# Kernel optimization log

Measured on AMD Instinct MI355X. Metric: run time of the kernel, lower is better.

## Reference

```python
import jax, jax.numpy as jnp
import numpy as np
from jax import lax

D_MODEL = 512
N_HEADS = 8
D_HEAD = D_MODEL // N_HEADS
MAX_LANDMARKS = 100


def setup_inputs() -> dict:
    key = jax.random.key(0)
    ks = jax.random.split(key, 12)
    B, L, D = 16, 8192, D_MODEL
    s = 1.0 / np.sqrt(D)
    return {
        "mamba_output": jax.random.normal(ks[0], (B, L, D), jnp.float32),
        "hawkes_skip": jax.random.normal(ks[1], (B, L, D), jnp.float32),
        "hawkes_weights": jax.random.uniform(ks[2], (B, L), jnp.float32),
        "Wq": jax.random.uniform(ks[3], (D, D), jnp.float32, -s, s),
        "bq": jax.random.uniform(ks[4], (D,), jnp.float32, -s, s),
        "Wk": jax.random.uniform(ks[5], (D, D), jnp.float32, -s, s),
        "bk": jax.random.uniform(ks[6], (D,), jnp.float32, -s, s),
        "Wv": jax.random.uniform(ks[7], (D, D), jnp.float32, -s, s),
        "bv": jax.random.uniform(ks[8], (D,), jnp.float32, -s, s),
        "Wo": jax.random.uniform(ks[9], (D, D), jnp.float32, -s, s),
        "bo": jax.random.uniform(ks[10], (D,), jnp.float32, -s, s),
    }


def reference(mamba_output, hawkes_skip, hawkes_weights,
              Wq, bq, Wk, bk, Wv, bv, Wo, bo):
    B, L, D = hawkes_skip.shape
    H, dh = N_HEADS, D_HEAD
    k = min(MAX_LANDMARKS, L)
    scale = dh ** (-0.5)

    # top-k landmark selection over sequence, then chronological sort
    _, idx = lax.top_k(hawkes_weights, k)          # (B, k)
    idx = jnp.sort(idx, axis=1)
    landmark_kv = jnp.take_along_axis(hawkes_skip, idx[:, :, None], axis=1)  # (B, k, D)

    # single query = last timestep of mamba output
    query = mamba_output[:, -1, :]                 # (B, D)
    Q = (query @ Wq.T + bq).reshape(B, H, dh)      # (B, H, dh)
    K = (landmark_kv @ Wk.T + bk).reshape(B, k, H, dh)
    V = (landmark_kv @ Wv.T + bv).reshape(B, k, H, dh)

    scores = jnp.einsum("bhd,bkhd->bhk", Q, K) * scale   # (B, H, k)
    probs = jax.nn.softmax(scores, axis=-1)
    attn = jnp.einsum("bhk,bkhd->bhd", probs, V).reshape(B, D)
    return attn @ Wo.T + bo                        # (B, D)
```

## Files before the change

kernel.cpp:

```cpp
#include <hip/hip_runtime.h>
#include <hip/hip_bf16.h>
#include <stdint.h>

#define B_SZ 16
#define L_SEQ 8192
#define D_MOD 512
#define N_H 8
#define D_H 64
#define KSEL 100

__global__ __launch_bounds__(256) void topk_kernel(const float* __restrict__ w,
                                                   int* __restrict__ idx_out) {
    const int b = blockIdx.x;
    const float* wb = w + (size_t)b * L_SEQ;
    __shared__ uint32_t uval[L_SEQ];
    __shared__ int hist[256];
    __shared__ uint32_t s_thresh;
    __shared__ int s_rem;
    __shared__ int s_cntgt;
    const int t = threadIdx.x;

    for (int i = t; i < L_SEQ; i += 256) uval[i] = __float_as_uint(wb[i]);

    uint32_t prefix = 0, pmask = 0;
    int remaining = KSEL;
    for (int pass = 0; pass < 4; ++pass) {
        const int shift = 24 - 8 * pass;
        hist[t] = 0;
        __syncthreads();
        for (int i = t; i < L_SEQ; i += 256) {
            uint32_t u = uval[i];
            if ((u & pmask) == prefix) atomicAdd(&hist[(u >> shift) & 0xFF], 1);
        }
        __syncthreads();
        if (t == 0) {
            int cum = 0;
            int bin = 255;
            for (; bin > 0; --bin) {
                int h = hist[bin];
                if (cum + h >= remaining) break;
                cum += h;
            }
            s_thresh = prefix | ((uint32_t)bin << shift);
            s_rem = remaining - cum;
        }
        __syncthreads();
        prefix = s_thresh;
        remaining = s_rem;
        pmask |= (uint32_t)0xFF << shift;
        __syncthreads();
    }

    if (t == 0) s_cntgt = 0;
    __syncthreads();
    int* out = idx_out + b * KSEL;
    for (int i = t; i < L_SEQ; i += 256) {
        if (uval[i] > prefix) {
            int p = atomicAdd(&s_cntgt, 1);
            out[p] = i;
        }
    }
    __syncthreads();
    const int cntgt = s_cntgt;
    if (t < 64) {
        int needed = remaining;
        int taken = 0;
        for (int base = 0; base < L_SEQ && needed > 0; base += 64) {
            bool eq = (uval[base + t] == prefix);
            unsigned long long mask = __ballot(eq);
            int before = __popcll(mask & ((1ull << t) - 1ull));
            int c = __popcll(mask);
            int take = c < needed ? c : needed;
            if (eq && before < take) out[cntgt + taken + before] = base + t;
            taken += take;
            needed -= take;
        }
    }
}

__global__ __launch_bounds__(256) void attn_kernel(
    const float* __restrict__ mamba, const float* __restrict__ skip,
    const float* __restrict__ Wq, const float* __restrict__ bq,
    const float* __restrict__ Wk, const float* __restrict__ bk,
    const float* __restrict__ Wv, const float* __restrict__ bv,
    const int* __restrict__ idx, float* __restrict__ attn_out) {
    const int b = blockIdx.x >> 3;
    const int h = blockIdx.x & 7;
    const int t = threadIdx.x;
    const int lane = t & 63;
    const int wave = t >> 6;

    __shared__ float s_query[D_MOD];
    __shared__ float s_Qh[D_H];
    __shared__ float s_a[D_MOD];
    __shared__ float s_scores[128];
    __shared__ float s_p[128];
    __shared__ float s_y[D_MOD];
    __shared__ int s_idx[KSEL];
    __shared__ float s_qdotbk;

    const float* q = mamba + ((size_t)b * L_SEQ + (L_SEQ - 1)) * D_MOD;
    for (int i = t; i < D_MOD; i += 256) s_query[i] = q[i];
    for (int i = t; i < KSEL; i += 256) s_idx[i] = idx[b * KSEL + i];
    __syncthreads();

    const float* Wqh = Wq + (size_t)(h * D_H) * D_MOD;
    for (int d = wave; d < D_H; d += 4) {
        const float4* row4 = (const float4*)(Wqh + (size_t)d * D_MOD);
        const float4* q4 = (const float4*)s_query;
        float4 w0 = row4[lane * 2], w1 = row4[lane * 2 + 1];
        float4 q0 = q4[lane * 2], q1 = q4[lane * 2 + 1];
        float sum = w0.x * q0.x + w0.y * q0.y + w0.z * q0.z + w0.w * q0.w +
                    w1.x * q1.x + w1.y * q1.y + w1.z * q1.z + w1.w * q1.w;
        #pragma unroll
        for (int off = 32; off > 0; off >>= 1) sum += __shfl_down(sum, off);
        if (lane == 0) s_Qh[d] = sum + bq[h * D_H + d];
    }
    __syncthreads();

    if (wave == 0) {
        float v = s_Qh[lane] * bk[h * D_H + lane];
        #pragma unroll
        for (int off = 32; off > 0; off >>= 1) v += __shfl_down(v, off);
        if (lane == 0) s_qdotbk = v;
    }

    const float* Wkh = Wk + (size_t)(h * D_H) * D_MOD;
    {
        float2 acc = {0.f, 0.f};
        #pragma unroll 8
        for (int d = 0; d < D_H; ++d) {
            float qd = s_Qh[d];
            float2 wv = ((const float2*)(Wkh + (size_t)d * D_MOD))[t];
            acc.x += qd * wv.x;
            acc.y += qd * wv.y;
        }
        s_a[2 * t] = acc.x;
        s_a[2 * t + 1] = acc.y;
    }
    __syncthreads();

    const float scale = 0.125f;
    for (int j = wave; j < KSEL; j += 4) {
        const float4* x4 =
            (const float4*)(skip + ((size_t)b * L_SEQ + s_idx[j]) * D_MOD);
        const float4* a4 = (const float4*)s_a;
        float4 xv0 = x4[lane * 2], xv1 = x4[lane * 2 + 1];
        float4 a0 = a4[lane * 2], a1 = a4[lane * 2 + 1];
        float sum = xv0.x * a0.x + xv0.y * a0.y + xv0.z * a0.z + xv0.w * a0.w +
                    xv1.x * a1.x + xv1.y * a1.y + xv1.z * a1.z + xv1.w * a1.w;
        #pragma unroll
        for (int off = 32; off > 0; off >>= 1) sum += __shfl_down(sum, off);
        if (lane == 0) s_scores[j] = (sum + s_qdotbk) * scale;
    }
    __syncthreads();

    if (wave == 0) {
        float v0 = (lane < KSEL) ? s_scores[lane] : -3.4e38f;
        float v1 = (lane + 64 < KSEL) ? s_scores[lane + 64] : -3.4e38f;
        float m = fmaxf(v0, v1);
        #pragma unroll
        for (int off = 32; off > 0; off >>= 1) m = fmaxf(m, __shfl_down(m, off));
        m = __shfl(m, 0);
        float e0 = (lane < KSEL) ? expf(v0 - m) : 0.f;
        float e1 = (lane + 64 < KSEL) ? expf(v1 - m) : 0.f;
        float s = e0 + e1;
        #pragma unroll
        for (int off = 32; off > 0; off >>= 1) s += __shfl_down(s, off);
        s = __shfl(s, 0);
        float inv = 1.f / s;
        if (lane < KSEL) s_p[lane] = e0 * inv;
        if (lane + 64 < KSEL) s_p[lane + 64] = e1 * inv;
    }
    __syncthreads();

    {
        float2 acc = {0.f, 0.f};
        for (int j = 0; j < KSEL; ++j) {
            float pj = s_p[j];
            float2 xv =
                ((const float2*)(skip + ((size_t)b * L_SEQ + s_idx[j]) * D_MOD))[t];
            acc.x += pj * xv.x;
            acc.y += pj * xv.y;
        }
        s_y[2 * t] = acc.x;
        s_y[2 * t + 1] = acc.y;
    }
    __syncthreads();

    const float* Wvh = Wv + (size_t)(h * D_H) * D_MOD;
    for (int d = wave; d < D_H; d += 4) {
        const float4* row4 = (const float4*)(Wvh + (size_t)d * D_MOD);
        const float4* y4 = (const float4*)s_y;
        float4 w0 = row4[lane * 2], w1 = row4[lane * 2 + 1];
        float4 y0 = y4[lane * 2], y1 = y4[lane * 2 + 1];
        float sum = w0.x * y0.x + w0.y * y0.y + w0.z * y0.z + w0.w * y0.w +
                    w1.x * y1.x + w1.y * y1.y + w1.z * y1.z + w1.w * y1.w;
        #pragma unroll
        for (int off = 32; off > 0; off >>= 1) sum += __shfl_down(sum, off);
        if (lane == 0) attn_out[(size_t)b * D_MOD + h * D_H + d] = sum + bv[h * D_H + d];
    }
}

__global__ __launch_bounds__(256) void out_kernel(const float* __restrict__ attn,
                                                  const float* __restrict__ Wo,
                                                  const float* __restrict__ bo,
                                                  float* __restrict__ out) {
    const int b = blockIdx.x & 15;
    const int rc = blockIdx.x >> 4;
    const int t = threadIdx.x;
    const int lane = t & 63;
    const int wave = t >> 6;

    __shared__ float s_attn[D_MOD];
    for (int i = t; i < D_MOD; i += 256) s_attn[i] = attn[(size_t)b * D_MOD + i];
    __syncthreads();

    for (int d = wave; d < 64; d += 4) {
        const int r = rc * 64 + d;
        const float4* row4 = (const float4*)(Wo + (size_t)r * D_MOD);
        const float4* a4 = (const float4*)s_attn;
        float4 w0 = row4[lane * 2], w1 = row4[lane * 2 + 1];
        float4 a0 = a4[lane * 2], a1 = a4[lane * 2 + 1];
        float sum = w0.x * a0.x + w0.y * a0.y + w0.z * a0.z + w0.w * a0.w +
                    w1.x * a1.x + w1.y * a1.y + w1.z * a1.z + w1.w * a1.w;
        #pragma unroll
        for (int off = 32; off > 0; off >>= 1) sum += __shfl_down(sum, off);
        if (lane == 0) out[(size_t)b * D_MOD + r] = sum + bo[r];
    }
}

extern "C" void kernel_launch(void* const* d_in, const int* in_sizes, int n_in,
                              void* d_out, int out_size, void* d_ws, size_t ws_size,
                              hipStream_t stream) {
    const float* mamba = (const float*)d_in[0];
    const float* skip  = (const float*)d_in[1];
    const float* hw    = (const float*)d_in[2];
    const float* Wq    = (const float*)d_in[3];
    const float* bq    = (const float*)d_in[4];
    const float* Wk    = (const float*)d_in[5];
    const float* bk    = (const float*)d_in[6];
    const float* Wv    = (const float*)d_in[7];
    const float* bv    = (const float*)d_in[8];
    const float* Wo    = (const float*)d_in[9];
    const float* bo    = (const float*)d_in[10];
    float* out = (float*)d_out;

    int* idx = (int*)d_ws;
    float* attn = (float*)((char*)d_ws + 8192);

    topk_kernel<<<B_SZ, 256, 0, stream>>>(hw, idx);
    attn_kernel<<<B_SZ * N_H, 256, 0, stream>>>(mamba, skip, Wq, bq, Wk, bk,
                                                Wv, bv, idx, attn);
    out_kernel<<<B_SZ * N_H, 256, 0, stream>>>(attn, Wo, bo, out);
}
```

Before: 528.9 us.

## Fuse top-k selection into attention kernel with single-pass online softmax

Removes the separate top-k kernel by having every (batch, head) block redo the radix-select over the batch's 8192 weights in shared memory, so the Q/K projection work overlaps with it and one launch and a global round trip go away. Blocks grow to 512 threads, the serial histogram scan becomes a parallel suffix-sum, and the score, softmax and weighted-sum stages merge into one online-softmax pass so each landmark row is read once instead of twice. The cost is that top-k is computed eight times per batch, and the larger shared footprint (about 50KB) lowers occupancy.

```diff
diff --git a/kernel.cpp b/kernel.cpp
--- a/kernel.cpp
+++ b/kernel.cpp
@@ -9,112 +9,52 @@
 #define D_H 64
 #define KSEL 100
 
-__global__ __launch_bounds__(256) void topk_kernel(const float* __restrict__ w,
-                                                   int* __restrict__ idx_out) {
-    const int b = blockIdx.x;
-    const float* wb = w + (size_t)b * L_SEQ;
-    __shared__ uint32_t uval[L_SEQ];
-    __shared__ int hist[256];
-    __shared__ uint32_t s_thresh;
-    __shared__ int s_rem;
-    __shared__ int s_cntgt;
-    const int t = threadIdx.x;
-
-    for (int i = t; i < L_SEQ; i += 256) uval[i] = __float_as_uint(wb[i]);
-
-    uint32_t prefix = 0, pmask = 0;
-    int remaining = KSEL;
-    for (int pass = 0; pass < 4; ++pass) {
-        const int shift = 24 - 8 * pass;
-        hist[t] = 0;
-        __syncthreads();
-        for (int i = t; i < L_SEQ; i += 256) {
-            uint32_t u = uval[i];
-            if ((u & pmask) == prefix) atomicAdd(&hist[(u >> shift) & 0xFF], 1);
-        }
-        __syncthreads();
-        if (t == 0) {
-            int cum = 0;
-            int bin = 255;
-            for (; bin > 0; --bin) {
-                int h = hist[bin];
-                if (cum + h >= remaining) break;
-                cum += h;
-            }
-            s_thresh = prefix | ((uint32_t)bin << shift);
-            s_rem = remaining - cum;
-        }
-        __syncthreads();
-        prefix = s_thresh;
-        remaining = s_rem;
-        pmask |= (uint32_t)0xFF << shift;
-        __syncthreads();
-    }
-
-    if (t == 0) s_cntgt = 0;
-    __syncthreads();
-    int* out = idx_out + b * KSEL;
-    for (int i = t; i < L_SEQ; i += 256) {
-        if (uval[i] > prefix) {
-            int p = atomicAdd(&s_cntgt, 1);
-            out[p] = i;
-        }
-    }
-    __syncthreads();
-    const int cntgt = s_cntgt;
-    if (t < 64) {
-        int needed = remaining;
-        int taken = 0;
-        for (int base = 0; base < L_SEQ && needed > 0; base += 64) {
-            bool eq = (uval[base + t] == prefix);
-            unsigned long long mask = __ballot(eq);
-            int before = __popcll(mask & ((1ull << t) - 1ull));
-            int c = __popcll(mask);
-            int take = c < needed ? c : needed;
-            if (eq && before < take) out[cntgt + taken + before] = base + t;
-            taken += take;
-            needed -= take;
-        }
-    }
-}
-
-__global__ __launch_bounds__(256) void attn_kernel(
+__global__ __launch_bounds__(512) void fused_attn_kernel(
     const float* __restrict__ mamba, const float* __restrict__ skip,
+    const float* __restrict__ w,
     const float* __restrict__ Wq, const float* __restrict__ bq,
     const float* __restrict__ Wk, const float* __restrict__ bk,
     const float* __restrict__ Wv, const float* __restrict__ bv,
-    const int* __restrict__ idx, float* __restrict__ attn_out) {
+    float* __restrict__ attn_out) {
     const int b = blockIdx.x >> 3;
     const int h = blockIdx.x & 7;
     const int t = threadIdx.x;
     const int lane = t & 63;
     const int wave = t >> 6;
 
+    __shared__ uint32_t uval[L_SEQ];
+    __shared__ float s_part[8 * D_MOD];
     __shared__ float s_query[D_MOD];
+    __shared__ float s_a[D_MOD];
+    __shared__ float s_y[D_MOD];
     __shared__ float s_Qh[D_H];
-    __shared__ float s_a[D_MOD];
-    __shared__ float s_scores[128];
-    __shared__ float s_p[128];
-    __shared__ float s_y[D_MOD];
-    __shared__ int s_idx[KSEL];
+    __shared__ int s_idx[128];
+    __shared__ int hist[256];
+    __shared__ int s_wtot[4];
+    __shared__ float s_m[8], s_l[8];
+    __shared__ uint32_t s_thresh;
+    __shared__ int s_rem, s_cnt;
     __shared__ float s_qdotbk;
 
-    const float* q = mamba + ((size_t)b * L_SEQ + (L_SEQ - 1)) * D_MOD;
-    for (int i = t; i < D_MOD; i += 256) s_query[i] = q[i];
-    for (int i = t; i < KSEL; i += 256) s_idx[i] = idx[b * KSEL + i];
+    const float* qrow = mamba + ((size_t)b * L_SEQ + (L_SEQ - 1)) * D_MOD;
+    if (t < D_MOD) s_query[t] = qrow[t];
+    const float* wb = w + (size_t)b * L_SEQ;
+    for (int i = t; i < L_SEQ; i += 512) uval[i] = __float_as_uint(wb[i]);
     __syncthreads();
 
     const float* Wqh = Wq + (size_t)(h * D_H) * D_MOD;
-    for (int d = wave; d < D_H; d += 4) {
-        const float4* row4 = (const float4*)(Wqh + (size_t)d * D_MOD);
+    {
         const float4* q4 = (const float4*)s_query;
-        float4 w0 = row4[lane * 2], w1 = row4[lane * 2 + 1];
         float4 q0 = q4[lane * 2], q1 = q4[lane * 2 + 1];
-        float sum = w0.x * q0.x + w0.y * q0.y + w0.z * q0.z + w0.w * q0.w +
-                    w1.x * q1.x + w1.y * q1.y + w1.z * q1.z + w1.w * q1.w;
-        #pragma unroll
-        for (int off = 32; off > 0; off >>= 1) sum += __shfl_down(sum, off);
-        if (lane == 0) s_Qh[d] = sum + bq[h * D_H + d];
+        for (int d = wave; d < D_H; d += 8) {
+            const float4* row4 = (const float4*)(Wqh + (size_t)d * D_MOD);
+            float4 w0 = row4[lane * 2], w1 = row4[lane * 2 + 1];
+            float sum = w0.x * q0.x + w0.y * q0.y + w0.z * q0.z + w0.w * q0.w +
+                        w1.x * q1.x + w1.y * q1.y + w1.z * q1.z + w1.w * q1.w;
+            #pragma unroll
+            for (int off = 32; off > 0; off >>= 1) sum += __shfl_down(sum, off);
+            if (lane == 0) s_Qh[d] = sum + bq[h * D_H + d];
+        }
     }
     __syncthreads();
 
@@ -124,81 +64,155 @@
         for (int off = 32; off > 0; off >>= 1) v += __shfl_down(v, off);
         if (lane == 0) s_qdotbk = v;
     }
-
-    const float* Wkh = Wk + (size_t)(h * D_H) * D_MOD;
-    {
-        float2 acc = {0.f, 0.f};
-        #pragma unroll 8
-        for (int d = 0; d < D_H; ++d) {
+    {
+        const float* Wkh = Wk + (size_t)(h * D_H) * D_MOD;
+        float4 a0 = {0, 0, 0, 0}, a1 = {0, 0, 0, 0};
+        #pragma unroll
+        for (int dd = 0; dd < 8; ++dd) {
+            const int d = wave * 8 + dd;
             float qd = s_Qh[d];
-            float2 wv = ((const float2*)(Wkh + (size_t)d * D_MOD))[t];
-            acc.x += qd * wv.x;
-            acc.y += qd * wv.y;
-        }
-        s_a[2 * t] = acc.x;
-        s_a[2 * t + 1] = acc.y;
+            const float4* row4 = (const float4*)(Wkh + (size_t)d * D_MOD);
+            float4 w0 = row4[lane * 2], w1 = row4[lane * 2 + 1];
+            a0.x += qd * w0.x; a0.y += qd * w0.y; a0.z += qd * w0.z; a0.w += qd * w0.w;
+            a1.x += qd * w1.x; a1.y += qd * w1.y; a1.z += qd * w1.z; a1.w += qd * w1.w;
+        }
+        float4* p4 = (float4*)&s_part[wave * D_MOD + lane * 8];
+        p4[0] = a0; p4[1] = a1;
+    }
+    __syncthreads();
+    {
+        float v = 0.f;
+        #pragma unroll
+        for (int ww = 0; ww < 8; ++ww) v += s_part[ww * D_MOD + t];
+        s_a[t] = v;
+    }
+
+    uint32_t prefix = 0, pmask = 0;
+    int remaining = KSEL;
+    for (int pass = 0; pass < 4; ++pass) {
+        const int shift = 24 - 8 * pass;
+        if (t < 256) hist[t] = 0;
+        __syncthreads();
+        for (int i = t; i < L_SEQ; i += 512) {
+            uint32_t u = uval[i];
+            if ((u & pmask) == prefix) atomicAdd(&hist[(u >> shift) & 0xFF], 1);
+        }
+        __syncthreads();
+        int v = 0;
+        if (t < 256) {
+            v = hist[t];
+            #pragma unroll
+            for (int off = 1; off < 64; off <<= 1) {
+                int u = __shfl_down(v, off);
+                if (lane + off < 64) v += u;
+            }
+            if (lane == 0) s_wtot[wave] = v;
+        }
+        __syncthreads();
+        if (t < 256) {
+            int hi = 0;
+            for (int w2 = wave + 1; w2 < 4; ++w2) hi += s_wtot[w2];
+            int suff = v + hi;
+            int suff_next = suff - hist[t];
+            if (suff >= remaining && suff_next < remaining) {
+                s_thresh = prefix | ((uint32_t)t << shift);
+                s_rem = remaining - suff_next;
+            }
+        }
+        __syncthreads();
+        prefix = s_thresh;
+        remaining = s_rem;
+        pmask |= (uint32_t)0xFF << shift;
+        __syncthreads();
+    }
+
+    if (t == 0) s_cnt = 0;
+    __syncthreads();
+    for (int i = t; i < L_SEQ; i += 512) {
+        if (uval[i] > prefix) {
+            int p = atomicAdd(&s_cnt, 1);
+            s_idx[p] = i;
+        }
+    }
+    __syncthreads();
+    const int cntgt = s_cnt;
+    if (wave == 0) {
+        int needed = remaining;
+        int taken = 0;
+        for (int base = 0; base < L_SEQ && needed > 0; base += 64) {
+            bool eq = (uval[base + lane] == prefix);
+            unsigned long long mask = __ballot(eq);
+            int before = __popcll(mask & ((1ull << lane) - 1ull));
+            int c = __popcll(mask);
+            int take = c < needed ? c : needed;
+            if (eq && before < take) s_idx[cntgt + taken + before] = base + lane;
+            taken += take;
+            needed -= take;
+        }
     }
     __syncthreads();
 
     const float scale = 0.125f;
-    for (int j = wave; j < KSEL; j += 4) {
-        const float4* x4 =
-            (const float4*)(skip + ((size_t)b * L_SEQ + s_idx[j]) * D_MOD);
+    {
         const float4* a4 = (const float4*)s_a;
-        float4 xv0 = x4[lane * 2], xv1 = x4[lane * 2 + 1];
-        float4 a0 = a4[lane * 2], a1 = a4[lane * 2 + 1];
-        float sum = xv0.x * a0.x + xv0.y * a0.y + xv0.z * a0.z + xv0.w * a0.w +
-                    xv1.x * a1.x + xv1.y * a1.y + xv1.z * a1.z + xv1.w * a1.w;
-        #pragma unroll
-        for (int off = 32; off > 0; off >>= 1) sum += __shfl_down(sum, off);
-        if (lane == 0) s_scores[j] = (sum + s_qdotbk) * scale;
-    }
-    __syncthreads();
-
-    if (wave == 0) {
-        float v0 = (lane < KSEL) ? s_scores[lane] : -3.4e38f;
-        float v1 = (lane + 64 < KSEL) ? s_scores[lane + 64] : -3.4e38f;
-        float m = fmaxf(v0, v1);
-        #pragma unroll
-        for (int off = 32; off > 0; off >>= 1) m = fmaxf(m, __shfl_down(m, off));
-        m = __shfl(m, 0);
-        float e0 = (lane < KSEL) ? expf(v0 - m) : 0.f;
-        float e1 = (lane + 64 < KSEL) ? expf(v1 - m) : 0.f;
-        float s = e0 + e1;
-        #pragma unroll
-        for (int off = 32; off > 0; off >>= 1) s += __shfl_down(s, off);
-        s = __shfl(s, 0);
-        float inv = 1.f / s;
-        if (lane < KSEL) s_p[lane] = e0 * inv;
-        if (lane + 64 < KSEL) s_p[lane + 64] = e1 * inv;
-    }
-    __syncthreads();
-
-    {
-        float2 acc = {0.f, 0.f};
-        for (int j = 0; j < KSEL; ++j) {
-            float pj = s_p[j];
-            float2 xv =
-                ((const float2*)(skip + ((size_t)b * L_SEQ + s_idx[j]) * D_MOD))[t];
-            acc.x += pj * xv.x;
-            acc.y += pj * xv.y;
-        }
-        s_y[2 * t] = acc.x;
-        s_y[2 * t + 1] = acc.y;
+        float4 av0 = a4[lane * 2], av1 = a4[lane * 2 + 1];
+        float qdotbk = s_qdotbk;
+        float m = -INFINITY, l = 0.f;
+        float4 acc0 = {0, 0, 0, 0}, acc1 = {0, 0, 0, 0};
+        for (int j = wave; j < KSEL; j += 8) {
+            const float4* x4 =
+                (const float4*)(skip + ((size_t)b * L_SEQ + s_idx[j]) * D_MOD);
+            float4 x0 = x4[lane * 2], x1 = x4[lane * 2 + 1];
+            float sum = x0.x * av0.x + x0.y * av0.y + x0.z * av0.z + x0.w * av0.w +
+                        x1.x * av1.x + x1.y * av1.y + x1.z * av1.z + x1.w * av1.w;
+            #pragma unroll
+            for (int off = 32; off > 0; off >>= 1) sum += __shfl_xor(sum, off);
+            float s = (sum + qdotbk) * scale;
+            float mnew = fmaxf(m, s);
+            float c = expf(m - mnew);
+            float e = expf(s - mnew);
+            l = l * c + e;
+            acc0.x = acc0.x * c + e * x0.x; acc0.y = acc0.y * c + e * x0.y;
+            acc0.z = acc0.z * c + e * x0.z; acc0.w = acc0.w * c + e * x0.w;
+            acc1.x = acc1.x * c + e * x1.x; acc1.y = acc1.y * c + e * x1.y;
+            acc1.z = acc1.z * c + e * x1.z; acc1.w = acc1.w * c + e * x1.w;
+            m = mnew;
+        }
+        float4* p4 = (float4*)&s_part[wave * D_MOD + lane * 8];
+        p4[0] = acc0; p4[1] = acc1;
+        if (lane == 0) { s_m[wave] = m; s_l[wave] = l; }
+    }
+    __syncthreads();
+
+    {
+        float mstar = -INFINITY;
+        #pragma unroll
+        for (int ww = 0; ww < 8; ++ww) mstar = fmaxf(mstar, s_m[ww]);
+        float num = 0.f, den = 0.f;
+        #pragma unroll
+        for (int ww = 0; ww < 8; ++ww) {
+            float sc = expf(s_m[ww] - mstar);
+            num += sc * s_part[ww * D_MOD + t];
+            den += sc * s_l[ww];
+        }
+        s_y[t] = num / den;
     }
     __syncthreads();
 
     const float* Wvh = Wv + (size_t)(h * D_H) * D_MOD;
-    for (int d = wave; d < D_H; d += 4) {
-        const float4* row4 = (const float4*)(Wvh + (size_t)d * D_MOD);
+    {
         const float4* y4 = (const float4*)s_y;
-        float4 w0 = row4[lane * 2], w1 = row4[lane * 2 + 1];
         float4 y0 = y4[lane * 2], y1 = y4[lane * 2 + 1];
-        float sum = w0.x * y0.x + w0.y * y0.y + w0.z * y0.z + w0.w * y0.w +
-                    w1.x * y1.x + w1.y * y1.y + w1.z * y1.z + w1.w * y1.w;
-        #pragma unroll
-        for (int off = 32; off > 0; off >>= 1) sum += __shfl_down(sum, off);
-        if (lane == 0) attn_out[(size_t)b * D_MOD + h * D_H + d] = sum + bv[h * D_H + d];
+        for (int d = wave; d < D_H; d += 8) {
+            const float4* row4 = (const float4*)(Wvh + (size_t)d * D_MOD);
+            float4 w0 = row4[lane * 2], w1 = row4[lane * 2 + 1];
+            float sum = w0.x * y0.x + w0.y * y0.y + w0.z * y0.z + w0.w * y0.w +
+                        w1.x * y1.x + w1.y * y1.y + w1.z * y1.z + w1.w * y1.w;
+            #pragma unroll
+            for (int off = 32; off > 0; off >>= 1) sum += __shfl_down(sum, off);
+            if (lane == 0)
+                attn_out[(size_t)b * D_MOD + h * D_H + d] = sum + bv[h * D_H + d];
+        }
     }
 }
 
@@ -216,12 +230,12 @@
     for (int i = t; i < D_MOD; i += 256) s_attn[i] = attn[(size_t)b * D_MOD + i];
     __syncthreads();
 
+    const float4* a4 = (const float4*)s_attn;
+    float4 a0 = a4[lane * 2], a1 = a4[lane * 2 + 1];
     for (int d = wave; d < 64; d += 4) {
         const int r = rc * 64 + d;
         const float4* row4 = (const float4*)(Wo + (size_t)r * D_MOD);
-        const float4* a4 = (const float4*)s_attn;
         float4 w0 = row4[lane * 2], w1 = row4[lane * 2 + 1];
-        float4 a0 = a4[lane * 2], a1 = a4[lane * 2 + 1];
         float sum = w0.x * a0.x + w0.y * a0.y + w0.z * a0.z + w0.w * a0.w +
                     w1.x * a1.x + w1.y * a1.y + w1.z * a1.z + w1.w * a1.w;
         #pragma unroll
@@ -246,11 +260,9 @@
     const float* bo    = (const float*)d_in[10];
     float* out = (float*)d_out;
 
-    int* idx = (int*)d_ws;
-    float* attn = (float*)((char*)d_ws + 8192);
-
-    topk_kernel<<<B_SZ, 256, 0, stream>>>(hw, idx);
-    attn_kernel<<<B_SZ * N_H, 256, 0, stream>>>(mamba, skip, Wq, bq, Wk, bk,
-                                                Wv, bv, idx, attn);
+    float* attn = (float*)d_ws;
+
+    fused_attn_kernel<<<B_SZ * N_H, 512, 0, stream>>>(mamba, skip, hw, Wq, bq,
+                                                      Wk, bk, Wv, bv, attn);
     out_kernel<<<B_SZ * N_H, 256, 0, stream>>>(attn, Wo, bo, out);
 }
```

After: 464.2 us. 12.2% less time.
